# Optimization experiments

Measured on AMD Instinct MI355X. Metric: run time of the kernel, lower is better.

## Reference

```python
import jax, jax.numpy as jnp
import numpy as np

NUM_NODES = 50000
FEAT_DIM = 256
CLIPS = 8
DIM = 128
K_NEIGH = 32
B, S = 2048, 10


def setup_inputs() -> dict:
    key = jax.random.key(0)
    k1, k2, k3, k4 = jax.random.split(key, 4)
    nodes = jax.random.randint(k1, (B, S), 0, NUM_NODES, dtype=jnp.int64)
    adj = jax.random.randint(k2, (NUM_NODES, K_NEIGH), 0, NUM_NODES, dtype=jnp.int64)
    features = jax.random.normal(k3, (NUM_NODES, FEAT_DIM), dtype=jnp.float32)
    # xavier-uniform-ish scale for local_weight [clips, dim, feat_dim]
    limit = float(np.sqrt(6.0 / (DIM + FEAT_DIM)))
    local_weight = jax.random.uniform(k4, (CLIPS, DIM, FEAT_DIM), dtype=jnp.float32,
                                      minval=-limit, maxval=limit)
    return {"nodes": nodes, "adj": adj, "features": features, "local_weight": local_weight}


def reference(nodes, adj, features, local_weight):
    # order == 1: one hop of mean aggregation over sampled neighbor lists
    nodes_flat = nodes.reshape(-1)                      # [n]
    neigh = adj[nodes_flat]                             # [n, K] irregular gather
    feat = features[neigh].mean(axis=1)                 # [n, d] gather + mean
    # einsum('ckd,dn->ckn').permute(2,0,1) == einsum('ckd,nd->nck')
    local_out = jnp.einsum('ckd,nd->nck', local_weight, feat)   # [n, clips, dim]
    local_embs = jax.nn.relu(local_out)
    return local_embs.reshape(nodes.shape[0], nodes.shape[1], local_weight.shape[0], -1)
```

## Files before the change

kernel.cpp:

```cpp
#include <hip/hip_runtime.h>

#define FEAT_DIM 256
#define K_NEIGH  32
#define NROWS    20480
#define NOUT     1024
#define NUM_NODES 50000
#define SLICE_DIM 32
#define NSLICE    8
#define FBLK      1563

typedef __attribute__((ext_vector_type(8))) short bf16x8;
typedef __attribute__((ext_vector_type(4))) float f32x4;

__device__ __forceinline__ unsigned short f2bf(float f) {
    unsigned int u = __builtin_bit_cast(unsigned int, f);
    u += 0x7fffu + ((u >> 16) & 1u);
    return (unsigned short)(u >> 16);
}
__device__ __forceinline__ float bf2f(unsigned short h) {
    unsigned int u = ((unsigned int)h) << 16;
    return __builtin_bit_cast(float, u);
}
__device__ __forceinline__ void gload16(const void* g, void* l) {
    __builtin_amdgcn_global_load_lds(
        (const __attribute__((address_space(1))) unsigned int*)g,
        (__attribute__((address_space(3))) unsigned int*)l, 16, 0, 0);
}

__global__ __launch_bounds__(256) void wcvt_kernel(const float* __restrict__ w,
                                                   unsigned short* __restrict__ wb) {
    int i = (blockIdx.x * 256 + threadIdx.x) * 4;
    float4 v = *(const float4*)(w + i);
    ushort4 o;
    o.x = f2bf(v.x); o.y = f2bf(v.y); o.z = f2bf(v.z); o.w = f2bf(v.w);
    *(ushort4*)(wb + i) = o;
}

__global__ __launch_bounds__(256) void cvt_kernel(const float* __restrict__ f,
                                                  unsigned short* __restrict__ fb,
                                                  const float* __restrict__ w,
                                                  unsigned short* __restrict__ wb) {
    int b = blockIdx.x;
    int t = threadIdx.x;
    if (b < FBLK) {
        int g = t >> 5;
        int i = t & 31;
        int node = b * 32 + i;
        if (node >= NUM_NODES) return;
        const float* src = f + (long)node * FEAT_DIM + g * SLICE_DIM;
        unsigned short o[32];
        #pragma unroll
        for (int j = 0; j < 32; j += 4) {
            float4 v = *(const float4*)(src + j);
            o[j] = f2bf(v.x); o[j+1] = f2bf(v.y); o[j+2] = f2bf(v.z); o[j+3] = f2bf(v.w);
        }
        unsigned short* dst = fb + ((long)g * NUM_NODES + node) * SLICE_DIM;
        #pragma unroll
        for (int j = 0; j < 4; ++j)
            *(bf16x8*)(dst + j * 8) = *(const bf16x8*)(o + j * 8);
    } else {
        int i = ((b - FBLK) * 256 + t) * 4;
        float4 v = *(const float4*)(w + i);
        ushort4 o;
        o.x = f2bf(v.x); o.y = f2bf(v.y); o.z = f2bf(v.z); o.w = f2bf(v.w);
        *(ushort4*)(wb + i) = o;
    }
}

__global__ __launch_bounds__(256) void agg_sliced(const int* __restrict__ nodes,
                                                  const int* __restrict__ adj,
                                                  const unsigned short* __restrict__ fb,
                                                  unsigned short* __restrict__ feat) {
    int slice = blockIdx.x & 7;
    int chunk = blockIdx.x >> 3;
    int t = threadIdx.x;
    int row = chunk * 64 + (t >> 2);
    int d8 = (t & 3) * 8;
    int node = nodes[row];
    const int* arow = adj + (long)node * K_NEIGH;
    int nbr[K_NEIGH];
    #pragma unroll
    for (int kk = 0; kk < K_NEIGH / 4; ++kk)
        *(int4*)(nbr + kk * 4) = ((const int4*)arow)[kk];

    const unsigned short* base = fb + (long)slice * NUM_NODES * SLICE_DIM + d8;
    float acc[8] = {};
    #pragma unroll
    for (int k = 0; k < K_NEIGH; ++k) {
        bf16x8 v = *(const bf16x8*)(base + (long)nbr[k] * SLICE_DIM);
        #pragma unroll
        for (int j = 0; j < 8; ++j) acc[j] += bf2f((unsigned short)v[j]);
    }
    unsigned short o[8];
    #pragma unroll
    for (int j = 0; j < 8; ++j) o[j] = f2bf(acc[j] * (1.0f / K_NEIGH));
    *(bf16x8*)(feat + (long)row * FEAT_DIM + slice * SLICE_DIM + d8) = *(const bf16x8*)o;
}

__global__ __launch_bounds__(256) void agg_f32_kernel(const int* __restrict__ nodes,
                                                      const int* __restrict__ adj,
                                                      const float* __restrict__ features,
                                                      unsigned short* __restrict__ feat) {
    int row = blockIdx.x;
    int t = threadIdx.x;
    int node = nodes[row];
    const int* arow = adj + (long)node * K_NEIGH;
    float acc = 0.f;
    #pragma unroll
    for (int k = 0; k < K_NEIGH; ++k) {
        long nb = arow[k];
        acc += features[nb * FEAT_DIM + t];
    }
    feat[(long)row * FEAT_DIM + t] = f2bf(acc * (1.0f / K_NEIGH));
}

__global__ __launch_bounds__(256) void gemm_kernel(const unsigned short* __restrict__ A,
                                                   const unsigned short* __restrict__ Bw,
                                                   float* __restrict__ C) {
    __shared__ short As[2][128 * 32];
    __shared__ short Bs[2][128 * 32];

    int t = threadIdx.x;
    int wave = t >> 6, lane = t & 63;
    int wm = wave >> 1, wn = wave & 1;
    int m0 = blockIdx.x * 128, n0 = blockIdx.y * 128;
    int lr = lane & 15;
    int lk = (lane >> 4) * 8;

    int srow = t >> 2;
    int sseg = (t & 3) * 8;
    const short* Ag = (const short*)A + (long)(m0 + srow) * FEAT_DIM + sseg;
    const short* Bg = (const short*)Bw + (long)(n0 + srow) * FEAT_DIM + sseg;

    f32x4 acc[4][4] = {};

#define STAGE(bufi, kb) do {                                         \
    gload16(Ag + (kb), &As[bufi][t * 8]);                            \
    gload16(Ag + 64 * FEAT_DIM + (kb), &As[bufi][64 * 32 + t * 8]);  \
    gload16(Bg + (kb), &Bs[bufi][t * 8]);                            \
    gload16(Bg + 64 * FEAT_DIM + (kb), &Bs[bufi][64 * 32 + t * 8]);  \
} while (0)

    STAGE(0, 0);
    asm volatile("s_waitcnt vmcnt(0)" ::: "memory");
    __builtin_amdgcn_s_barrier();

    #pragma unroll
    for (int it = 0; it < 8; ++it) {
        int cur = it & 1;
        if (it < 7) STAGE(cur ^ 1, (it + 1) * 32);

        bf16x8 a[4], b[4];
        #pragma unroll
        for (int i = 0; i < 4; ++i)
            a[i] = *(const bf16x8*)(&As[cur][(wm * 64 + i * 16 + lr) * 32 + lk]);
        #pragma unroll
        for (int j = 0; j < 4; ++j)
            b[j] = *(const bf16x8*)(&Bs[cur][(wn * 64 + j * 16 + lr) * 32 + lk]);
        #pragma unroll
        for (int i = 0; i < 4; ++i)
            #pragma unroll
            for (int j = 0; j < 4; ++j)
                acc[i][j] = __builtin_amdgcn_mfma_f32_16x16x32_bf16(a[i], b[j], acc[i][j], 0, 0, 0);

        if (it < 7) {
            asm volatile("s_waitcnt vmcnt(0)" ::: "memory");
            __builtin_amdgcn_s_barrier();
        }
    }
#undef STAGE

    int crow0 = m0 + wm * 64 + (lane >> 4) * 4;
    int ccol0 = n0 + wn * 64 + lr;
    #pragma unroll
    for (int i = 0; i < 4; ++i)
        #pragma unroll
        for (int j = 0; j < 4; ++j)
            #pragma unroll
            for (int r = 0; r < 4; ++r) {
                float v = acc[i][j][r];
                C[(long)(crow0 + i * 16 + r) * NOUT + ccol0 + j * 16] = v > 0.f ? v : 0.f;
            }
}

extern "C" void kernel_launch(void* const* d_in, const int* in_sizes, int n_in,
                              void* d_out, int out_size, void* d_ws, size_t ws_size,
                              hipStream_t stream) {
    const int*   nodes    = (const int*)d_in[0];
    const int*   adj      = (const int*)d_in[1];
    const float* features = (const float*)d_in[2];
    const float* lw       = (const float*)d_in[3];
    float*       out      = (float*)d_out;

    const size_t fbf_elems  = (size_t)NUM_NODES * FEAT_DIM;
    const size_t feat_elems = (size_t)NROWS * FEAT_DIM;
    const size_t need = (fbf_elems + feat_elems + (size_t)NOUT * FEAT_DIM) * 2;

    if (ws_size >= need) {
        unsigned short* fbf  = (unsigned short*)d_ws;
        unsigned short* feat = fbf + fbf_elems;
        unsigned short* wb   = feat + feat_elems;

        cvt_kernel<<<FBLK + (NOUT * FEAT_DIM) / (256 * 4), 256, 0, stream>>>(features, fbf, lw, wb);
        agg_sliced<<<(NROWS / 64) * NSLICE, 256, 0, stream>>>(nodes, adj, fbf, feat);
        gemm_kernel<<<dim3(NROWS / 128, NOUT / 128), 256, 0, stream>>>(feat, wb, out);
    } else {
        unsigned short* feat = (unsigned short*)d_ws;
        unsigned short* wb   = feat + feat_elems;

        wcvt_kernel<<<(NOUT * FEAT_DIM) / (256 * 4), 256, 0, stream>>>(lw, wb);
        agg_f32_kernel<<<NROWS, 256, 0, stream>>>(nodes, adj, features, feat);
        gemm_kernel<<<dim3(NROWS / 128, NOUT / 128), 256, 0, stream>>>(feat, wb, out);
    }
}
```

Measured before the change: 78.16 us.

## Fuse neighbor aggregation into GEMM with per-block LDS staging of aggregated rows

Replaces the separate aggregation and GEMM kernels with one fused kernel. Each block aggregates 32 rows (one thread per row-slice) into a swizzled LDS tile, then computes the full 1024-wide output row block, reading bf16 weights directly from global memory. Output is written with nontemporal stores. This removes the intermediate feature buffer round-trip and one launch, but each block re-reads the full weight matrix from global/L2 and uses only 640 blocks with heavy register use (32-wide accumulators, 32 MFMA tiles per wave). The fallback GEMM also loses its double buffering.

Result: slower. 166.8 us (+113.4%).

```diff
diff --git a/kernel.cpp b/kernel.cpp
--- a/kernel.cpp
+++ b/kernel.cpp
@@ -8,9 +8,11 @@
 #define SLICE_DIM 32
 #define NSLICE    8
 #define FBLK      1563
+#define MT        32
 
 typedef __attribute__((ext_vector_type(8))) short bf16x8;
 typedef __attribute__((ext_vector_type(4))) float f32x4;
+typedef __attribute__((ext_vector_type(4))) int   i32x4;
 
 __device__ __forceinline__ unsigned short f2bf(float f) {
     unsigned int u = __builtin_bit_cast(unsigned int, f);
@@ -20,11 +22,6 @@
 __device__ __forceinline__ float bf2f(unsigned short h) {
     unsigned int u = ((unsigned int)h) << 16;
     return __builtin_bit_cast(float, u);
-}
-__device__ __forceinline__ void gload16(const void* g, void* l) {
-    __builtin_amdgcn_global_load_lds(
-        (const __attribute__((address_space(1))) unsigned int*)g,
-        (__attribute__((address_space(3))) unsigned int*)l, 16, 0, 0);
 }
 
 __global__ __launch_bounds__(256) void wcvt_kernel(const float* __restrict__ w,
@@ -67,34 +64,85 @@
     }
 }
 
-__global__ __launch_bounds__(256) void agg_sliced(const int* __restrict__ nodes,
-                                                  const int* __restrict__ adj,
-                                                  const unsigned short* __restrict__ fb,
-                                                  unsigned short* __restrict__ feat) {
-    int slice = blockIdx.x & 7;
-    int chunk = blockIdx.x >> 3;
-    int t = threadIdx.x;
-    int row = chunk * 64 + (t >> 2);
-    int d8 = (t & 3) * 8;
-    int node = nodes[row];
-    const int* arow = adj + (long)node * K_NEIGH;
-    int nbr[K_NEIGH];
-    #pragma unroll
-    for (int kk = 0; kk < K_NEIGH / 4; ++kk)
-        *(int4*)(nbr + kk * 4) = ((const int4*)arow)[kk];
-
-    const unsigned short* base = fb + (long)slice * NUM_NODES * SLICE_DIM + d8;
-    float acc[8] = {};
-    #pragma unroll
-    for (int k = 0; k < K_NEIGH; ++k) {
-        bf16x8 v = *(const bf16x8*)(base + (long)nbr[k] * SLICE_DIM);
-        #pragma unroll
-        for (int j = 0; j < 8; ++j) acc[j] += bf2f((unsigned short)v[j]);
-    }
-    unsigned short o[8];
-    #pragma unroll
-    for (int j = 0; j < 8; ++j) o[j] = f2bf(acc[j] * (1.0f / K_NEIGH));
-    *(bf16x8*)(feat + (long)row * FEAT_DIM + slice * SLICE_DIM + d8) = *(const bf16x8*)o;
+__global__ __launch_bounds__(256) void fused_kernel(const int* __restrict__ nodes,
+                                                    const int* __restrict__ adj,
+                                                    const unsigned short* __restrict__ fb,
+                                                    const unsigned short* __restrict__ wb,
+                                                    float* __restrict__ C) {
+    __shared__ short As[MT * FEAT_DIM];
+
+    int t = threadIdx.x;
+    int m0 = blockIdx.x * MT;
+
+    {
+        int row = t >> 3;
+        int slice = t & 7;
+        int node = nodes[m0 + row];
+        const int* arow = adj + (long)node * K_NEIGH;
+        int nbr[K_NEIGH];
+        #pragma unroll
+        for (int kk = 0; kk < K_NEIGH / 4; ++kk) {
+            i32x4 q = *(const i32x4*)(arow + kk * 4);
+            nbr[kk*4] = q.x; nbr[kk*4+1] = q.y; nbr[kk*4+2] = q.z; nbr[kk*4+3] = q.w;
+        }
+        const unsigned short* base = fb + (long)slice * NUM_NODES * SLICE_DIM;
+        float acc[32] = {};
+        #pragma unroll 4
+        for (int k = 0; k < K_NEIGH; ++k) {
+            const unsigned short* p = base + (long)nbr[k] * SLICE_DIM;
+            #pragma unroll
+            for (int q4 = 0; q4 < 4; ++q4) {
+                bf16x8 v = *(const bf16x8*)(p + q4 * 8);
+                #pragma unroll
+                for (int j = 0; j < 8; ++j) acc[q4 * 8 + j] += bf2f((unsigned short)v[j]);
+            }
+        }
+        char* rowp = (char*)As + row * (FEAT_DIM * 2);
+        #pragma unroll
+        for (int q4 = 0; q4 < 4; ++q4) {
+            unsigned short o[8];
+            #pragma unroll
+            for (int j = 0; j < 8; ++j) o[j] = f2bf(acc[q4 * 8 + j] * (1.0f / K_NEIGH));
+            int byte_in_row = (slice * 64 + q4 * 16) ^ ((row & 7) << 4);
+            *(bf16x8*)(rowp + byte_in_row) = *(const bf16x8*)o;
+        }
+    }
+    __syncthreads();
+
+    int wave = t >> 6, lane = t & 63;
+    int lr = lane & 15;
+    int lk = (lane >> 4) * 8;
+    const short* Bg = (const short*)wb + (long)(wave * 256 + lr) * FEAT_DIM + lk;
+
+    f32x4 acc2[2][16] = {};
+    #pragma unroll
+    for (int kb = 0; kb < FEAT_DIM; kb += 32) {
+        bf16x8 a[2];
+        #pragma unroll
+        for (int mf = 0; mf < 2; ++mf) {
+            int row = mf * 16 + lr;
+            int byte_in_row = ((kb + lk) * 2) ^ ((row & 7) << 4);
+            a[mf] = *(const bf16x8*)((const char*)As + row * (FEAT_DIM * 2) + byte_in_row);
+        }
+        #pragma unroll
+        for (int nf = 0; nf < 16; ++nf) {
+            bf16x8 b = *(const bf16x8*)(Bg + (long)nf * 16 * FEAT_DIM + kb);
+            acc2[0][nf] = __builtin_amdgcn_mfma_f32_16x16x32_bf16(a[0], b, acc2[0][nf], 0, 0, 0);
+            acc2[1][nf] = __builtin_amdgcn_mfma_f32_16x16x32_bf16(a[1], b, acc2[1][nf], 0, 0, 0);
+        }
+    }
+
+    #pragma unroll
+    for (int mf = 0; mf < 2; ++mf)
+        #pragma unroll
+        for (int nf = 0; nf < 16; ++nf)
+            #pragma unroll
+            for (int r = 0; r < 4; ++r) {
+                int crow = m0 + mf * 16 + (lane >> 4) * 4 + r;
+                int ccol = wave * 256 + nf * 16 + lr;
+                float v = acc2[mf][nf][r];
+                __builtin_nontemporal_store(v > 0.f ? v : 0.f, &C[(long)crow * NOUT + ccol]);
+            }
 }
 
 __global__ __launch_bounds__(256) void agg_f32_kernel(const int* __restrict__ nodes,
@@ -117,59 +165,37 @@
 __global__ __launch_bounds__(256) void gemm_kernel(const unsigned short* __restrict__ A,
                                                    const unsigned short* __restrict__ Bw,
                                                    float* __restrict__ C) {
-    __shared__ short As[2][128 * 32];
-    __shared__ short Bs[2][128 * 32];
-
+    __shared__ short As2[128 * 32];
+    __shared__ short Bs2[128 * 32];
     int t = threadIdx.x;
     int wave = t >> 6, lane = t & 63;
     int wm = wave >> 1, wn = wave & 1;
     int m0 = blockIdx.x * 128, n0 = blockIdx.y * 128;
-    int lr = lane & 15;
-    int lk = (lane >> 4) * 8;
-
-    int srow = t >> 2;
-    int sseg = (t & 3) * 8;
+    int lr = lane & 15, lk = (lane >> 4) * 8;
+    int srow = t >> 2, sseg = (t & 3) * 8;
     const short* Ag = (const short*)A + (long)(m0 + srow) * FEAT_DIM + sseg;
     const short* Bg = (const short*)Bw + (long)(n0 + srow) * FEAT_DIM + sseg;
-
     f32x4 acc[4][4] = {};
-
-#define STAGE(bufi, kb) do {                                         \
-    gload16(Ag + (kb), &As[bufi][t * 8]);                            \
-    gload16(Ag + 64 * FEAT_DIM + (kb), &As[bufi][64 * 32 + t * 8]);  \
-    gload16(Bg + (kb), &Bs[bufi][t * 8]);                            \
-    gload16(Bg + 64 * FEAT_DIM + (kb), &Bs[bufi][64 * 32 + t * 8]);  \
-} while (0)
-
-    STAGE(0, 0);
-    asm volatile("s_waitcnt vmcnt(0)" ::: "memory");
-    __builtin_amdgcn_s_barrier();
-
-    #pragma unroll
-    for (int it = 0; it < 8; ++it) {
-        int cur = it & 1;
-        if (it < 7) STAGE(cur ^ 1, (it + 1) * 32);
-
+    for (int kb = 0; kb < FEAT_DIM; kb += 32) {
+        if (kb) __syncthreads();
+        *(bf16x8*)&As2[t * 8] = *(const bf16x8*)(Ag + kb);
+        *(bf16x8*)&As2[64 * 32 + t * 8] = *(const bf16x8*)(Ag + 64 * FEAT_DIM + kb);
+        *(bf16x8*)&Bs2[t * 8] = *(const bf16x8*)(Bg + kb);
+        *(bf16x8*)&Bs2[64 * 32 + t * 8] = *(const bf16x8*)(Bg + 64 * FEAT_DIM + kb);
+        __syncthreads();
         bf16x8 a[4], b[4];
         #pragma unroll
         for (int i = 0; i < 4; ++i)
-            a[i] = *(const bf16x8*)(&As[cur][(wm * 64 + i * 16 + lr) * 32 + lk]);
+            a[i] = *(const bf16x8*)(&As2[(wm * 64 + i * 16 + lr) * 32 + lk]);
         #pragma unroll
         for (int j = 0; j < 4; ++j)
-            b[j] = *(const bf16x8*)(&Bs[cur][(wn * 64 + j * 16 + lr) * 32 + lk]);
+            b[j] = *(const bf16x8*)(&Bs2[(wn * 64 + j * 16 + lr) * 32 + lk]);
         #pragma unroll
         for (int i = 0; i < 4; ++i)
             #pragma unroll
             for (int j = 0; j < 4; ++j)
                 acc[i][j] = __builtin_amdgcn_mfma_f32_16x16x32_bf16(a[i], b[j], acc[i][j], 0, 0, 0);
-
-        if (it < 7) {
-            asm volatile("s_waitcnt vmcnt(0)" ::: "memory");
-            __builtin_amdgcn_s_barrier();
-        }
-    }
-#undef STAGE
-
+    }
     int crow0 = m0 + wm * 64 + (lane >> 4) * 4;
     int ccol0 = n0 + wn * 64 + lr;
     #pragma unroll
@@ -193,17 +219,16 @@
     float*       out      = (float*)d_out;
 
     const size_t fbf_elems  = (size_t)NUM_NODES * FEAT_DIM;
+    const size_t wb_elems   = (size_t)NOUT * FEAT_DIM;
     const size_t feat_elems = (size_t)NROWS * FEAT_DIM;
-    const size_t need = (fbf_elems + feat_elems + (size_t)NOUT * FEAT_DIM) * 2;
+    const size_t need = (fbf_elems + wb_elems) * 2;
 
     if (ws_size >= need) {
-        unsigned short* fbf  = (unsigned short*)d_ws;
-        unsigned short* feat = fbf + fbf_elems;
-        unsigned short* wb   = feat + feat_elems;
+        unsigned short* fbf = (unsigned short*)d_ws;
+        unsigned short* wb  = fbf + fbf_elems;
 
         cvt_kernel<<<FBLK + (NOUT * FEAT_DIM) / (256 * 4), 256, 0, stream>>>(features, fbf, lw, wb);
-        agg_sliced<<<(NROWS / 64) * NSLICE, 256, 0, stream>>>(nodes, adj, fbf, feat);
-        gemm_kernel<<<dim3(NROWS / 128, NOUT / 128), 256, 0, stream>>>(feat, wb, out);
+        fused_kernel<<<NROWS / MT, 256, 0, stream>>>(nodes, adj, fbf, wb, out);
     } else {
         unsigned short* feat = (unsigned short*)d_ws;
         unsigned short* wb   = feat + feat_elems;
```
